# Performance work log

Measured on AMD Instinct MI355X. Metric: run time of the kernel, lower is better.

The kernel has to match this reference:

```python
import jax, jax.numpy as jnp
import numpy as np

# SGCN (AsynSpiGCN) internals are not in the source; reconstructed as a standard
# LIF spiking-GCN: per time step, spikes propagate along edges weighted by
# edge_attr (gather src -> scatter-add dst), membrane potential decays with
# decay_alpha, neurons fire above threshold unless refractory, reset to v_r.
V_REST = 0.0
V_R = 0.0
SPEED = 1.0
THRESH = 0.5
REFRAC = 2.0
DECAY = 0.8
T_STEPS = 8
BETA = 0.5

N_NODES = 50000
N_EDGES = 800000
IN_DIM = 256
HID_DIM = 128


def setup_inputs() -> dict:
    key = jax.random.key(0)
    k1, k2, k3, k4, k5 = jax.random.split(key, 5)
    x = jax.random.normal(k1, (N_NODES, IN_DIM), dtype=jnp.float32)
    spike_node = jax.random.randint(k2, (N_NODES,), 0, 2, dtype=jnp.int32)
    edge_index = jax.random.randint(k3, (2, N_EDGES), 0, N_NODES, dtype=jnp.int32)
    node_indices = jnp.arange(N_NODES, dtype=jnp.int32)
    edge_attr = jax.random.uniform(k4, (N_EDGES,), dtype=jnp.float32)
    W = jax.random.normal(k5, (IN_DIM, HID_DIM), dtype=jnp.float32) * 0.05
    b = jnp.zeros((HID_DIM,), dtype=jnp.float32)
    return {"x": x, "spike_node": spike_node, "edge_index": edge_index,
            "node_indices": node_indices, "edge_attr": edge_attr, "W": W, "b": b}


def reference(x, spike_node, edge_index, node_indices, edge_attr, W, b):
    N = x.shape[0]
    # Linear projection + per-feature min-max standardization over nodes (dim 0)
    h = x @ W + b
    mn = h.min(axis=0, keepdims=True)
    mx = h.max(axis=0, keepdims=True)
    h = (h - mn) / (mx - mn + 1e-6)

    src, dst = edge_index[0], edge_index[1]
    v0 = jnp.full_like(h, V_REST)            # membrane potential [N, H]
    ref0 = jnp.zeros_like(h)                 # refractory counters [N, H]
    s0 = jnp.broadcast_to(spike_node.astype(h.dtype)[:, None], h.shape)

    def step(carry, _):
        v, ref, s = carry
        msg = s[src] * edge_attr[:, None]                      # [E, H] gather
        agg = jax.ops.segment_sum(msg, dst, num_segments=N)    # [N, H] scatter-add
        v = DECAY * v + SPEED * h + agg
        can_fire = ref <= 0
        spk = ((v >= THRESH) & can_fire).astype(h.dtype)
        v = jnp.where(spk > 0, V_R, v)
        ref = jnp.where(spk > 0, REFRAC, jnp.maximum(ref - 1.0, 0.0))
        return (v, ref, spk), spk

    (vT, _, _), spike_matrix = jax.lax.scan(step, (v0, ref0, s0), None, length=T_STEPS)
    fusion_tensor = h + BETA * vT
    return fusion_tensor, spike_matrix
```

## Files before the change

### kernel.cpp

```cpp
#include <hip/hip_runtime.h>
#include <cstdint>

#define N_NODES 50000
#define N_EDGES 800000
#define IN_DIM  256
#define HID     128
#define T_STEPS 8

static __device__ __forceinline__ unsigned int enc_f(float f) {
    unsigned int u = __float_as_uint(f);
    return (u & 0x80000000u) ? ~u : (u | 0x80000000u);
}
static __device__ __forceinline__ float dec_f(unsigned int u) {
    unsigned int b = (u & 0x80000000u) ? (u ^ 0x80000000u) : ~u;
    return __uint_as_float(b);
}

__global__ void k_count(const int* __restrict__ dst, int* __restrict__ counts) {
    int e = blockIdx.x * blockDim.x + threadIdx.x;
    if (e < N_EDGES) atomicAdd(&counts[dst[e]], 1);
}

__global__ void k_scan1(const int* __restrict__ counts, int* __restrict__ row_tmp,
                        int* __restrict__ blocksum) {
    __shared__ int sh[256];
    int t = threadIdx.x, i = blockIdx.x * 256 + t;
    int c = (i < N_NODES) ? counts[i] : 0;
    sh[t] = c; __syncthreads();
    for (int off = 1; off < 256; off <<= 1) {
        int val = (t >= off) ? sh[t - off] : 0;
        __syncthreads();
        sh[t] += val;
        __syncthreads();
    }
    if (i < N_NODES) row_tmp[i] = sh[t] - c;
    if (t == 255) blocksum[blockIdx.x] = sh[255];
}

__global__ void k_scan2(const int* __restrict__ blocksum, int* __restrict__ blockoff,
                        int nb, int* __restrict__ row_ptr) {
    if (threadIdx.x == 0) {
        int acc = 0;
        for (int b = 0; b < nb; ++b) { blockoff[b] = acc; acc += blocksum[b]; }
        row_ptr[N_NODES] = acc;
    }
}

__global__ void k_scan3(const int* __restrict__ row_tmp, const int* __restrict__ blockoff,
                        int* __restrict__ row_ptr) {
    int i = blockIdx.x * blockDim.x + threadIdx.x;
    if (i < N_NODES) row_ptr[i] = row_tmp[i] + blockoff[i >> 8];
}

__global__ void k_fill(const int* __restrict__ dst, const int* __restrict__ src,
                       const float* __restrict__ attr,
                       const int* __restrict__ row_ptr, int* __restrict__ cursor,
                       int* __restrict__ eid, int* __restrict__ src_s,
                       float* __restrict__ attr_s) {
    int e = blockIdx.x * blockDim.x + threadIdx.x;
    if (e >= N_EDGES) return;
    int d = dst[e];
    int p = row_ptr[d] + atomicAdd(&cursor[d], 1);
    eid[p]    = e;
    src_s[p]  = src[e];
    attr_s[p] = attr[e];
}

__global__ __launch_bounds__(256) void k_bsort(const int* __restrict__ row_ptr,
                                               int* __restrict__ eid,
                                               int* __restrict__ src_s,
                                               float* __restrict__ attr_s) {
    int node = blockIdx.x * 4 + (threadIdx.x >> 6);
    int l = threadIdx.x & 63;
    int beg = row_ptr[node], end = row_ptr[node + 1], cnt = end - beg;
    if (cnt <= 1) return;
    if (cnt <= 64) {
        int key = 0x7FFFFFFF, sv = 0; float av = 0.f;
        if (l < cnt) { key = eid[beg + l]; sv = src_s[beg + l]; av = attr_s[beg + l]; }
        #pragma unroll
        for (int k = 2; k <= 64; k <<= 1) {
            for (int j = k >> 1; j > 0; j >>= 1) {
                int   pk = __shfl_xor(key, j);
                int   ps = __shfl_xor(sv, j);
                float pa = __shfl_xor(av, j);
                bool lower = (l & j) == 0;
                bool asc   = (l & k) == 0;
                bool take_min = (lower == asc);
                bool take = take_min ? (pk < key) : (pk > key);
                if (take) { key = pk; sv = ps; av = pa; }
            }
        }
        if (l < cnt) { eid[beg + l] = key; src_s[beg + l] = sv; attr_s[beg + l] = av; }
    } else if (l == 0) {
        for (int i = beg + 1; i < end; ++i) {
            int ke = eid[i]; int ks = src_s[i]; float ka = attr_s[i];
            int m = i - 1;
            while (m >= beg && eid[m] > ke) {
                eid[m+1] = eid[m]; src_s[m+1] = src_s[m]; attr_s[m+1] = attr_s[m]; --m;
            }
            eid[m+1] = ke; src_s[m+1] = ks; attr_s[m+1] = ka;
        }
    }
}

__global__ __launch_bounds__(256) void k_gemm(const float* __restrict__ x,
                                              const float* __restrict__ W,
                                              const float* __restrict__ b,
                                              float* __restrict__ h,
                                              unsigned int* __restrict__ mn_e,
                                              unsigned int* __restrict__ mx_e) {
    __shared__ float Ws[32 * 128];
    __shared__ float xs[64 * 36];
    __shared__ float red_mn[8 * 128];
    __shared__ float red_mx[8 * 128];
    const int tid = threadIdx.x;
    const int n0 = blockIdx.x * 64;
    const int jt = tid & 31, nt = tid >> 5;
    const int j0 = jt * 4;

    float acc[8][4];
    #pragma unroll
    for (int a = 0; a < 8; ++a)
        #pragma unroll
        for (int c = 0; c < 4; ++c) acc[a][c] = 0.0f;

    const int ldn = tid >> 2;
    const int kq  = (tid & 3) * 8;
    const int xrow = (n0 + ldn < N_NODES) ? (n0 + ldn) : (N_NODES - 1);
    const float* xg = x + (size_t)xrow * IN_DIM;

    for (int kc = 0; kc < IN_DIM; kc += 32) {
        __syncthreads();
        float4 xa = *(const float4*)(xg + kc + kq);
        float4 xb = *(const float4*)(xg + kc + kq + 4);
        *(float4*)&xs[ldn * 36 + kq]     = xa;
        *(float4*)&xs[ldn * 36 + kq + 4] = xb;
        #pragma unroll
        for (int p = 0; p < 4; ++p) {
            int r = nt + p * 8;
            *(float4*)&Ws[r * 128 + j0] =
                *(const float4*)(W + (size_t)(kc + r) * HID + j0);
        }
        __syncthreads();
        const float* xbase = &xs[nt * 8 * 36];
        #pragma unroll 4
        for (int k = 0; k < 32; ++k) {
            float4 wf = *(const float4*)&Ws[k * 128 + j0];
            #pragma unroll
            for (int ni = 0; ni < 8; ++ni) {
                float xv = xbase[ni * 36 + k];
                acc[ni][0] = __fmaf_rn(xv, wf.x, acc[ni][0]);
                acc[ni][1] = __fmaf_rn(xv, wf.y, acc[ni][1]);
                acc[ni][2] = __fmaf_rn(xv, wf.z, acc[ni][2]);
                acc[ni][3] = __fmaf_rn(xv, wf.w, acc[ni][3]);
            }
        }
    }

    float4 bv = *(const float4*)(b + j0);
    float lmn[4], lmx[4];
    #pragma unroll
    for (int c = 0; c < 4; ++c) { lmn[c] = INFINITY; lmx[c] = -INFINITY; }
    #pragma unroll
    for (int ni = 0; ni < 8; ++ni) {
        acc[ni][0] = __fadd_rn(acc[ni][0], bv.x);
        acc[ni][1] = __fadd_rn(acc[ni][1], bv.y);
        acc[ni][2] = __fadd_rn(acc[ni][2], bv.z);
        acc[ni][3] = __fadd_rn(acc[ni][3], bv.w);
        #pragma unroll
        for (int c = 0; c < 4; ++c) {
            lmn[c] = fminf(lmn[c], acc[ni][c]);
            lmx[c] = fmaxf(lmx[c], acc[ni][c]);
        }
    }
    #pragma unroll
    for (int c = 0; c < 4; ++c) {
        red_mn[nt * 128 + j0 + c] = lmn[c];
        red_mx[nt * 128 + j0 + c] = lmx[c];
    }
    __syncthreads();
    if (tid < 128) {
        float mnv = red_mn[tid], mxv = red_mx[tid];
        #pragma unroll
        for (int r = 1; r < 8; ++r) {
            mnv = fminf(mnv, red_mn[r * 128 + tid]);
            mxv = fmaxf(mxv, red_mx[r * 128 + tid]);
        }
        atomicMin(&mn_e[tid], enc_f(mnv));
        atomicMax(&mx_e[tid], enc_f(mxv));
    }
    #pragma unroll
    for (int ni = 0; ni < 8; ++ni) {
        int n = n0 + nt * 8 + ni;
        if (n < N_NODES)
            *(float4*)&h[(size_t)n * HID + j0] =
                make_float4(acc[ni][0], acc[ni][1], acc[ni][2], acc[ni][3]);
    }
}

__global__ void k_init_bits(const int* __restrict__ spike_node, uint32_t* __restrict__ sb) {
    int n = blockIdx.x * blockDim.x + threadIdx.x;
    if (n >= N_NODES) return;
    uint32_t f = spike_node[n] ? 0xFFFFFFFFu : 0u;
    sb[(size_t)n * 4 + 0] = f;
    sb[(size_t)n * 4 + 1] = f;
    sb[(size_t)n * 4 + 2] = f;
    sb[(size_t)n * 4 + 3] = f;
}

__global__ __launch_bounds__(128) void k_step(const int* __restrict__ row_ptr,
                                              const int* __restrict__ src_s,
                                              const float* __restrict__ attr_s,
                                              const uint32_t* __restrict__ sb_cur,
                                              uint32_t* __restrict__ sb_nxt,
                                              float* __restrict__ h,
                                              float* __restrict__ v,
                                              unsigned char* __restrict__ refc,
                                              const unsigned int* __restrict__ mn_e,
                                              const unsigned int* __restrict__ mx_e,
                                              float* __restrict__ out_spk,
                                              float* __restrict__ out_fus,
                                              int t0, int is_last) {
    __shared__ float    attr_l[4][128];
    __shared__ uint32_t words_l[4][128][4];
    __shared__ uint32_t sbw[16];
    __shared__ int      rp[5];

    const int tid = threadIdx.x;
    const int ns = tid >> 5, ln = tid & 31;
    const int nb = blockIdx.x * 4;
    const int n  = nb + ns;

    if (tid < 16) sbw[tid] = 0;
    if (tid < 5)  rp[tid] = row_ptr[nb + tid];
    __syncthreads();

    const int beg = rp[ns], cnt = rp[ns + 1] - beg;
    int cmax = 0;
    #pragma unroll
    for (int q = 0; q < 4; ++q) cmax = max(cmax, rp[q + 1] - rp[q]);
    const int nchunk = (cmax + 127) >> 7;

    float agg0 = 0.f, agg1 = 0.f, agg2 = 0.f, agg3 = 0.f;
    const int w = ln >> 3, shb = (ln & 7) * 4;

    for (int ch = 0; ch < nchunk; ++ch) {
        int base = ch << 7;
        __syncthreads();
        #pragma unroll
        for (int rep = 0; rep < 4; ++rep) {
            int i = base + rep * 32 + ln;
            if (i < cnt) {
                int e = beg + i;
                int s = src_s[e];
                attr_l[ns][rep * 32 + ln] = attr_s[e];
                *(uint4*)&words_l[ns][rep * 32 + ln][0] =
                    *(const uint4*)&sb_cur[(size_t)s * 4];
            }
        }
        __syncthreads();
        int lim = min(128, cnt - base);
        for (int i = 0; i < lim; ++i) {
            uint32_t u = words_l[ns][i][w];
            float a = attr_l[ns][i];
            uint32_t bits = (u >> shb) & 0xFu;
            agg0 = __fadd_rn(agg0, (bits & 1u) ? a : 0.0f);
            agg1 = __fadd_rn(agg1, (bits & 2u) ? a : 0.0f);
            agg2 = __fadd_rn(agg2, (bits & 4u) ? a : 0.0f);
            agg3 = __fadd_rn(agg3, (bits & 8u) ? a : 0.0f);
        }
    }

    const size_t idx = (size_t)n * HID + ln * 4;
    float4 h4 = *(const float4*)&h[idx];
    if (t0) {
        const int jb = ln * 4;
        float hq[4] = {h4.x, h4.y, h4.z, h4.w};
        #pragma unroll
        for (int q = 0; q < 4; ++q) {
            float mn = dec_f(mn_e[jb + q]);
            float mx = dec_f(mx_e[jb + q]);
            float d2 = __fadd_rn(__fsub_rn(mx, mn), 1e-6f);
            hq[q] = __fdiv_rn(__fsub_rn(hq[q], mn), d2);
        }
        h4 = make_float4(hq[0], hq[1], hq[2], hq[3]);
        *(float4*)&h[idx] = h4;
    }
    float4 v4;
    unsigned int rcu;
    if (t0) { v4 = make_float4(0.f, 0.f, 0.f, 0.f); rcu = 0u; }
    else    { v4 = *(const float4*)&v[idx]; rcu = *(const unsigned int*)&refc[idx]; }

    float hv[4]  = {h4.x, h4.y, h4.z, h4.w};
    float vv[4]  = {v4.x, v4.y, v4.z, v4.w};
    float ag[4]  = {agg0, agg1, agg2, agg3};
    float vf[4], sf[4];
    unsigned int rcn = 0u, nib = 0u;
    #pragma unroll
    for (int q = 0; q < 4; ++q) {
        float vn = __fadd_rn(__fadd_rn(__fmul_rn(0.8f, vv[q]), hv[q]), ag[q]);
        unsigned int rc = (rcu >> (8 * q)) & 0xFFu;
        bool spk = (vn >= 0.5f) && (rc == 0u);
        vf[q] = spk ? 0.0f : vn;
        sf[q] = spk ? 1.0f : 0.0f;
        unsigned int rnew = spk ? 2u : (rc > 0u ? rc - 1u : 0u);
        rcn |= rnew << (8 * q);
        nib |= (spk ? 1u : 0u) << q;
    }
    *(float4*)&v[idx] = make_float4(vf[0], vf[1], vf[2], vf[3]);
    *(unsigned int*)&refc[idx] = rcn;
    *(float4*)&out_spk[idx] = make_float4(sf[0], sf[1], sf[2], sf[3]);
    if (is_last) {
        *(float4*)&out_fus[idx] = make_float4(
            __fadd_rn(hv[0], __fmul_rn(0.5f, vf[0])),
            __fadd_rn(hv[1], __fmul_rn(0.5f, vf[1])),
            __fadd_rn(hv[2], __fmul_rn(0.5f, vf[2])),
            __fadd_rn(hv[3], __fmul_rn(0.5f, vf[3])));
    }
    atomicOr(&sbw[ns * 4 + w], nib << shb);
    __syncthreads();
    if (tid < 16)
        sb_nxt[(size_t)(nb + (tid >> 2)) * 4 + (tid & 3)] = sbw[tid];
}

extern "C" void kernel_launch(void* const* d_in, const int* in_sizes, int n_in,
                              void* d_out, int out_size, void* d_ws, size_t ws_size,
                              hipStream_t stream) {
    const float* x          = (const float*)d_in[0];
    const int*   spike_node = (const int*)  d_in[1];
    const int*   edge_index = (const int*)  d_in[2];
    const float* edge_attr  = (const float*)d_in[4];
    const float* W          = (const float*)d_in[5];
    const float* b          = (const float*)d_in[6];
    float* out = (float*)d_out;

    const int* src = edge_index;
    const int* dst = edge_index + N_EDGES;

    char* wsp = (char*)d_ws;
    auto alloc = [&](size_t bytes) {
        char* p = wsp;
        wsp += (bytes + 255) & ~(size_t)255;
        return p;
    };
    float*         h        = (float*)        alloc((size_t)N_NODES * HID * 4);
    float*         v        = (float*)        alloc((size_t)N_NODES * HID * 4);
    unsigned char* refc     = (unsigned char*)alloc((size_t)N_NODES * HID);
    uint32_t*      sbA      = (uint32_t*)     alloc((size_t)N_NODES * 16);
    uint32_t*      sbB      = (uint32_t*)     alloc((size_t)N_NODES * 16);
    int*           counts   = (int*)          alloc((size_t)N_NODES * 4);
    int*           cursor   = (int*)          alloc((size_t)N_NODES * 4);
    int*           row_tmp  = (int*)          alloc((size_t)N_NODES * 4);
    int*           row_ptr  = (int*)          alloc((size_t)(N_NODES + 1) * 4);
    int*           blocksum = (int*)          alloc(256 * 4);
    int*           blockoff = (int*)          alloc(256 * 4);
    int*           eid      = (int*)          alloc((size_t)N_EDGES * 4);
    int*           src_s    = (int*)          alloc((size_t)N_EDGES * 4);
    float*         attr_s   = (float*)        alloc((size_t)N_EDGES * 4);
    unsigned int*  mn_e     = (unsigned int*) alloc(HID * 4);
    unsigned int*  mx_e     = (unsigned int*) alloc(HID * 4);

    hipMemsetAsync(counts, 0x00, (size_t)N_NODES * 4, stream);
    hipMemsetAsync(cursor, 0x00, (size_t)N_NODES * 4, stream);
    hipMemsetAsync(mn_e,   0xFF, HID * 4, stream);
    hipMemsetAsync(mx_e,   0x00, HID * 4, stream);

    const int NB = (N_NODES + 255) / 256;
    const int EB = (N_EDGES + 255) / 256;

    k_count<<<EB, 256, 0, stream>>>(dst, counts);
    k_scan1<<<NB, 256, 0, stream>>>(counts, row_tmp, blocksum);
    k_scan2<<<1, 64, 0, stream>>>(blocksum, blockoff, NB, row_ptr);
    k_scan3<<<NB, 256, 0, stream>>>(row_tmp, blockoff, row_ptr);
    k_fill<<<EB, 256, 0, stream>>>(dst, src, edge_attr, row_ptr, cursor, eid, src_s, attr_s);
    k_bsort<<<N_NODES / 4, 256, 0, stream>>>(row_ptr, eid, src_s, attr_s);

    k_gemm<<<(N_NODES + 63) / 64, 256, 0, stream>>>(x, W, b, h, mn_e, mx_e);
    k_init_bits<<<NB, 256, 0, stream>>>(spike_node, sbA);

    const size_t NH = (size_t)N_NODES * HID;
    for (int t = 0; t < T_STEPS; ++t) {
        uint32_t* cur = (t & 1) ? sbB : sbA;
        uint32_t* nxt = (t & 1) ? sbA : sbB;
        k_step<<<N_NODES / 4, 128, 0, stream>>>(row_ptr, src_s, attr_s, cur, nxt,
                                                h, v, refc, mn_e, mx_e,
                                                out + NH + (size_t)t * NH,
                                                out, (t == 0) ? 1 : 0,
                                                (t == T_STEPS - 1) ? 1 : 0);
    }
}
```

Before: 640.9 us.

## Fuse all spiking time steps into one persistent cooperative kernel

Replaces the eight per-step launches with one cooperative kernel that runs every LIF time step and uses grid.sync between steps. Each block owns 66 nodes and keeps their normalized h, membrane potential and refractory counters in registers. Its CSR edge slice is cached in LDS when it fits, so v, refc and h are no longer re-read from and written back to global memory each step. The cost is seven grid-wide barriers and a residency requirement that all ~758 blocks fit at once; if the occupancy check or the cooperative launch fails, the old per-step loop runs instead.

```diff
diff --git a/kernel.cpp b/kernel.cpp
--- a/kernel.cpp
+++ b/kernel.cpp
@@ -1,5 +1,8 @@
 #include <hip/hip_runtime.h>
+#include <hip/hip_cooperative_groups.h>
 #include <cstdint>
+
+namespace cg = cooperative_groups;
 
 #define N_NODES 50000
 #define N_EDGES 800000
@@ -321,6 +324,186 @@
     __syncthreads();
     if (tid < 16)
         sb_nxt[(size_t)(nb + (tid >> 2)) * 4 + (tid & 3)] = sbw[tid];
+}
+
+#define NPB 66
+#define ECAP 2048
+#define NSLOT 9
+#define GRID_F ((N_NODES + NPB - 1) / NPB)
+__global__ __launch_bounds__(256, 3) void k_fused(
+    const int* __restrict__ row_ptr,
+    const int* __restrict__ src_s,
+    const float* __restrict__ attr_s,
+    uint32_t* __restrict__ sbA,
+    uint32_t* __restrict__ sbB,
+    const float* __restrict__ h_raw,
+    const unsigned int* __restrict__ mn_e,
+    const unsigned int* __restrict__ mx_e,
+    float* __restrict__ out)
+{
+    __shared__ int      lrp[NPB + 1];
+    __shared__ int      ed_src[ECAP];
+    __shared__ float    ed_attr[ECAP];
+    __shared__ uint32_t sbw[NPB][4];
+
+    cg::grid_group grid = cg::this_grid();
+
+    const int tid = threadIdx.x;
+    const int g   = tid >> 5;
+    const int ln  = tid & 31;
+    const int n0  = blockIdx.x * NPB;
+    const int ncnt = (N_NODES - n0 < NPB) ? (N_NODES - n0) : NPB;
+    const int nwords = (ncnt > 0 ? ncnt : 0) * 4;
+    const int w = ln >> 3, shb = (ln & 7) * 4;
+    const size_t NH = (size_t)N_NODES * HID;
+
+    int ebase = 0; bool inlds = false;
+    if (ncnt > 0) {
+        if (tid <= ncnt) lrp[tid] = row_ptr[n0 + tid];
+        __syncthreads();
+        ebase = lrp[0];
+        int etot = lrp[ncnt] - ebase;
+        inlds = (etot <= ECAP);
+        if (inlds) {
+            for (int i = tid; i < etot; i += 256) {
+                ed_src[i]  = src_s[ebase + i];
+                ed_attr[i] = attr_s[ebase + i];
+            }
+        }
+    }
+    __syncthreads();
+
+    uint4 mnu = *(const uint4*)&mn_e[ln * 4];
+    uint4 mxu = *(const uint4*)&mx_e[ln * 4];
+    float mn0 = dec_f(mnu.x), mn1 = dec_f(mnu.y), mn2 = dec_f(mnu.z), mn3 = dec_f(mnu.w);
+    float dd0 = __fadd_rn(__fsub_rn(dec_f(mxu.x), mn0), 1e-6f);
+    float dd1 = __fadd_rn(__fsub_rn(dec_f(mxu.y), mn1), 1e-6f);
+    float dd2 = __fadd_rn(__fsub_rn(dec_f(mxu.z), mn2), 1e-6f);
+    float dd3 = __fadd_rn(__fsub_rn(dec_f(mxu.w), mn3), 1e-6f);
+
+    float4 hs[NSLOT], vs[NSLOT];
+    uint32_t rcs[NSLOT];
+    #pragma unroll
+    for (int s = 0; s < NSLOT; ++s) {
+        hs[s] = make_float4(0.f, 0.f, 0.f, 0.f);
+        vs[s] = make_float4(0.f, 0.f, 0.f, 0.f);
+        rcs[s] = 0u;
+        int m = s * 8 + g;
+        if (m < ncnt) {
+            size_t idx = (size_t)(n0 + m) * HID + ln * 4;
+            float4 t = *(const float4*)&h_raw[idx];
+            t.x = __fdiv_rn(__fsub_rn(t.x, mn0), dd0);
+            t.y = __fdiv_rn(__fsub_rn(t.y, mn1), dd1);
+            t.z = __fdiv_rn(__fsub_rn(t.z, mn2), dd2);
+            t.w = __fdiv_rn(__fsub_rn(t.w, mn3), dd3);
+            hs[s] = t;
+        }
+    }
+
+    for (int t = 0; t < T_STEPS; ++t) {
+        const uint32_t* cur = (t & 1) ? sbB : sbA;
+        uint32_t*       nxt = (t & 1) ? sbA : sbB;
+        if (t > 0) {
+            __threadfence();
+            grid.sync();
+            __threadfence();
+        }
+        for (int i2 = tid; i2 < nwords; i2 += 256) ((uint32_t*)sbw)[i2] = 0u;
+        __syncthreads();
+
+        #pragma unroll 1
+        for (int s = 0; s < NSLOT; ++s) {
+            int m = s * 8 + g;
+            if (m >= ncnt) continue;
+            int lb, le;
+            if (inlds) { lb = lrp[m] - ebase; le = lrp[m + 1] - ebase; }
+            else       { lb = lrp[m];         le = lrp[m + 1]; }
+            float ag0 = 0.f, ag1 = 0.f, ag2 = 0.f, ag3 = 0.f;
+            int i = lb;
+            if (inlds) {
+                for (; i + 3 < le; i += 4) {
+                    int e0 = ed_src[i], e1 = ed_src[i+1], e2 = ed_src[i+2], e3 = ed_src[i+3];
+                    uint32_t u0 = cur[(size_t)e0 * 4 + w];
+                    uint32_t u1 = cur[(size_t)e1 * 4 + w];
+                    uint32_t u2 = cur[(size_t)e2 * 4 + w];
+                    uint32_t u3 = cur[(size_t)e3 * 4 + w];
+                    float a0 = ed_attr[i], a1 = ed_attr[i+1], a2 = ed_attr[i+2], a3 = ed_attr[i+3];
+                    uint32_t b0 = (u0 >> shb) & 0xFu, b1 = (u1 >> shb) & 0xFu;
+                    uint32_t b2 = (u2 >> shb) & 0xFu, b3 = (u3 >> shb) & 0xFu;
+                    ag0 = __fadd_rn(ag0, (b0 & 1u) ? a0 : 0.f);
+                    ag1 = __fadd_rn(ag1, (b0 & 2u) ? a0 : 0.f);
+                    ag2 = __fadd_rn(ag2, (b0 & 4u) ? a0 : 0.f);
+                    ag3 = __fadd_rn(ag3, (b0 & 8u) ? a0 : 0.f);
+                    ag0 = __fadd_rn(ag0, (b1 & 1u) ? a1 : 0.f);
+                    ag1 = __fadd_rn(ag1, (b1 & 2u) ? a1 : 0.f);
+                    ag2 = __fadd_rn(ag2, (b1 & 4u) ? a1 : 0.f);
+                    ag3 = __fadd_rn(ag3, (b1 & 8u) ? a1 : 0.f);
+                    ag0 = __fadd_rn(ag0, (b2 & 1u) ? a2 : 0.f);
+                    ag1 = __fadd_rn(ag1, (b2 & 2u) ? a2 : 0.f);
+                    ag2 = __fadd_rn(ag2, (b2 & 4u) ? a2 : 0.f);
+                    ag3 = __fadd_rn(ag3, (b2 & 8u) ? a2 : 0.f);
+                    ag0 = __fadd_rn(ag0, (b3 & 1u) ? a3 : 0.f);
+                    ag1 = __fadd_rn(ag1, (b3 & 2u) ? a3 : 0.f);
+                    ag2 = __fadd_rn(ag2, (b3 & 4u) ? a3 : 0.f);
+                    ag3 = __fadd_rn(ag3, (b3 & 8u) ? a3 : 0.f);
+                }
+                for (; i < le; ++i) {
+                    int e0 = ed_src[i];
+                    uint32_t u0 = cur[(size_t)e0 * 4 + w];
+                    float a0 = ed_attr[i];
+                    uint32_t b0 = (u0 >> shb) & 0xFu;
+                    ag0 = __fadd_rn(ag0, (b0 & 1u) ? a0 : 0.f);
+                    ag1 = __fadd_rn(ag1, (b0 & 2u) ? a0 : 0.f);
+                    ag2 = __fadd_rn(ag2, (b0 & 4u) ? a0 : 0.f);
+                    ag3 = __fadd_rn(ag3, (b0 & 8u) ? a0 : 0.f);
+                }
+            } else {
+                for (; i < le; ++i) {
+                    int e0 = src_s[i];
+                    uint32_t u0 = cur[(size_t)e0 * 4 + w];
+                    float a0 = attr_s[i];
+                    uint32_t b0 = (u0 >> shb) & 0xFu;
+                    ag0 = __fadd_rn(ag0, (b0 & 1u) ? a0 : 0.f);
+                    ag1 = __fadd_rn(ag1, (b0 & 2u) ? a0 : 0.f);
+                    ag2 = __fadd_rn(ag2, (b0 & 4u) ? a0 : 0.f);
+                    ag3 = __fadd_rn(ag3, (b0 & 8u) ? a0 : 0.f);
+                }
+            }
+
+            float hv[4] = {hs[s].x, hs[s].y, hs[s].z, hs[s].w};
+            float vv[4] = {vs[s].x, vs[s].y, vs[s].z, vs[s].w};
+            float ag[4] = {ag0, ag1, ag2, ag3};
+            float vf[4], sf[4];
+            uint32_t rcu = rcs[s], rcn = 0u, nib = 0u;
+            #pragma unroll
+            for (int q = 0; q < 4; ++q) {
+                float vn = __fadd_rn(__fadd_rn(__fmul_rn(0.8f, vv[q]), hv[q]), ag[q]);
+                uint32_t rc = (rcu >> (8 * q)) & 0xFFu;
+                bool spk = (vn >= 0.5f) && (rc == 0u);
+                vf[q] = spk ? 0.0f : vn;
+                sf[q] = spk ? 1.0f : 0.0f;
+                uint32_t rnew = spk ? 2u : (rc > 0u ? rc - 1u : 0u);
+                rcn |= rnew << (8 * q);
+                nib |= (spk ? 1u : 0u) << q;
+            }
+            vs[s] = make_float4(vf[0], vf[1], vf[2], vf[3]);
+            rcs[s] = rcn;
+            size_t idx = (size_t)(n0 + m) * HID + ln * 4;
+            *(float4*)&out[NH + (size_t)t * NH + idx] =
+                make_float4(sf[0], sf[1], sf[2], sf[3]);
+            if (t == T_STEPS - 1) {
+                *(float4*)&out[idx] = make_float4(
+                    __fadd_rn(hv[0], __fmul_rn(0.5f, vf[0])),
+                    __fadd_rn(hv[1], __fmul_rn(0.5f, vf[1])),
+                    __fadd_rn(hv[2], __fmul_rn(0.5f, vf[2])),
+                    __fadd_rn(hv[3], __fmul_rn(0.5f, vf[3])));
+            }
+            atomicOr(&sbw[m][w], nib << shb);
+        }
+        __syncthreads();
+        for (int i2 = tid; i2 < nwords; i2 += 256)
+            nxt[(size_t)n0 * 4 + i2] = ((uint32_t*)sbw)[i2];
+    }
 }
 
 extern "C" void kernel_launch(void* const* d_in, const int* in_sizes, int n_in,
@@ -379,13 +562,37 @@
     k_init_bits<<<NB, 256, 0, stream>>>(spike_node, sbA);
 
     const size_t NH = (size_t)N_NODES * HID;
-    for (int t = 0; t < T_STEPS; ++t) {
-        uint32_t* cur = (t & 1) ? sbB : sbA;
-        uint32_t* nxt = (t & 1) ? sbA : sbB;
-        k_step<<<N_NODES / 4, 128, 0, stream>>>(row_ptr, src_s, attr_s, cur, nxt,
-                                                h, v, refc, mn_e, mx_e,
-                                                out + NH + (size_t)t * NH,
-                                                out, (t == 0) ? 1 : 0,
-                                                (t == T_STEPS - 1) ? 1 : 0);
-    }
-}
+
+    int maxB = 0;
+    hipError_t qerr = hipOccupancyMaxActiveBlocksPerMultiprocessor(&maxB, k_fused, 256, 0);
+    bool coop_done = false;
+    if (qerr == hipSuccess && maxB * 256 >= GRID_F) {
+        const int*          a_row  = row_ptr;
+        const int*          a_src  = src_s;
+        const float*        a_attr = attr_s;
+        uint32_t*           a_sbA  = sbA;
+        uint32_t*           a_sbB  = sbB;
+        const float*        a_h    = h;
+        const unsigned int* a_mn   = mn_e;
+        const unsigned int* a_mx   = mx_e;
+        float*              a_out  = out;
+        void* kargs[] = { (void*)&a_row, (void*)&a_src, (void*)&a_attr,
+                          (void*)&a_sbA, (void*)&a_sbB, (void*)&a_h,
+                          (void*)&a_mn,  (void*)&a_mx,  (void*)&a_out };
+        hipError_t lerr = hipLaunchCooperativeKernel((const void*)k_fused,
+                                                     dim3(GRID_F), dim3(256),
+                                                     kargs, 0, stream);
+        coop_done = (lerr == hipSuccess);
+    }
+    if (!coop_done) {
+        for (int t = 0; t < T_STEPS; ++t) {
+            uint32_t* cur = (t & 1) ? sbB : sbA;
+            uint32_t* nxt = (t & 1) ? sbA : sbB;
+            k_step<<<N_NODES / 4, 128, 0, stream>>>(row_ptr, src_s, attr_s, cur, nxt,
+                                                    h, v, refc, mn_e, mx_e,
+                                                    out + NH + (size_t)t * NH,
+                                                    out, (t == 0) ? 1 : 0,
+                                                    (t == T_STEPS - 1) ? 1 : 0);
+        }
+    }
+}
```

New measurement: 2.307 ms. 260% more time.

## Fuse all LIF time steps into one persistent kernel with grid barrier

Applied to the files above, without the earlier changes.

Replaces eight per-step kernel launches with a single persistent kernel of about 511 blocks. Each block owns 98 nodes and keeps h, v and refractory state in registers across steps. The block's edge lists are cached in LDS once, and steps are separated by a software global barrier built on atomics. This removes the global-memory round trips of v and refc, the repeated edge-list loads, and the launch overhead. The grid barrier depends on every block being co-resident (256 threads, launch_bounds 2 blocks/CU, heavy LDS and register use), so it risks deadlock or spilling, and the barrier adds serialization per step.

```diff
diff --git a/kernel.cpp b/kernel.cpp
--- a/kernel.cpp
+++ b/kernel.cpp
@@ -208,119 +208,176 @@
     sb[(size_t)n * 4 + 3] = f;
 }
 
-__global__ __launch_bounds__(128) void k_step(const int* __restrict__ row_ptr,
-                                              const int* __restrict__ src_s,
-                                              const float* __restrict__ attr_s,
-                                              const uint32_t* __restrict__ sb_cur,
-                                              uint32_t* __restrict__ sb_nxt,
-                                              float* __restrict__ h,
-                                              float* __restrict__ v,
-                                              unsigned char* __restrict__ refc,
-                                              const unsigned int* __restrict__ mn_e,
-                                              const unsigned int* __restrict__ mx_e,
-                                              float* __restrict__ out_spk,
-                                              float* __restrict__ out_fus,
-                                              int t0, int is_last) {
-    __shared__ float    attr_l[4][128];
-    __shared__ uint32_t words_l[4][128][4];
-    __shared__ uint32_t sbw[16];
-    __shared__ int      rp[5];
+static __device__ __forceinline__ void gbar(int* cnt, int* gen, int nblk) {
+    __syncthreads();
+    if (threadIdx.x == 0) {
+        __threadfence();
+        int g = __hip_atomic_load(gen, __ATOMIC_RELAXED, __HIP_MEMORY_SCOPE_AGENT);
+        int arrived = __hip_atomic_fetch_add(cnt, 1, __ATOMIC_ACQ_REL,
+                                             __HIP_MEMORY_SCOPE_AGENT);
+        if (arrived == nblk - 1) {
+            __hip_atomic_store(cnt, 0, __ATOMIC_RELAXED, __HIP_MEMORY_SCOPE_AGENT);
+            __threadfence();
+            __hip_atomic_fetch_add(gen, 1, __ATOMIC_ACQ_REL, __HIP_MEMORY_SCOPE_AGENT);
+        } else {
+            while (__hip_atomic_load(gen, __ATOMIC_RELAXED,
+                                     __HIP_MEMORY_SCOPE_AGENT) == g)
+                __builtin_amdgcn_s_sleep(16);
+        }
+        __threadfence();
+    }
+    __syncthreads();
+}
+
+#define NPB   98
+#define NSLOT 13
+#define ECAP  2048
+#define GRID_P ((N_NODES + NPB - 1) / NPB)
+__global__ __launch_bounds__(256, 2) void k_lif(
+    const int* __restrict__ row_ptr,
+    const int* __restrict__ src_s,
+    const float* __restrict__ attr_s,
+    uint32_t* __restrict__ sbA,
+    uint32_t* __restrict__ sbB,
+    const float* __restrict__ h_raw,
+    const unsigned int* __restrict__ mn_e,
+    const unsigned int* __restrict__ mx_e,
+    float* __restrict__ out,
+    int* __restrict__ bar_cnt,
+    int* __restrict__ bar_gen)
+{
+    __shared__ int      lrp[NPB + 1];
+    __shared__ int      ed_src_l[ECAP];
+    __shared__ float    ed_attr_l[ECAP];
+    __shared__ uint32_t ed_wds[ECAP * 4];
+    __shared__ uint32_t sbw[NPB][4];
 
     const int tid = threadIdx.x;
-    const int ns = tid >> 5, ln = tid & 31;
-    const int nb = blockIdx.x * 4;
-    const int n  = nb + ns;
-
-    if (tid < 16) sbw[tid] = 0;
-    if (tid < 5)  rp[tid] = row_ptr[nb + tid];
+    const int g   = tid >> 5;
+    const int ln  = tid & 31;
+    const int n0  = blockIdx.x * NPB;
+    const int ncnt = min(NPB, N_NODES - n0);
+    const int w = ln >> 3, shb = (ln & 7) * 4;
+    const size_t NH = (size_t)N_NODES * HID;
+
+    if (tid <= ncnt) lrp[tid] = row_ptr[n0 + tid];
     __syncthreads();
-
-    const int beg = rp[ns], cnt = rp[ns + 1] - beg;
-    int cmax = 0;
-    #pragma unroll
-    for (int q = 0; q < 4; ++q) cmax = max(cmax, rp[q + 1] - rp[q]);
-    const int nchunk = (cmax + 127) >> 7;
-
-    float agg0 = 0.f, agg1 = 0.f, agg2 = 0.f, agg3 = 0.f;
-    const int w = ln >> 3, shb = (ln & 7) * 4;
-
-    for (int ch = 0; ch < nchunk; ++ch) {
-        int base = ch << 7;
-        __syncthreads();
-        #pragma unroll
-        for (int rep = 0; rep < 4; ++rep) {
-            int i = base + rep * 32 + ln;
-            if (i < cnt) {
-                int e = beg + i;
-                int s = src_s[e];
-                attr_l[ns][rep * 32 + ln] = attr_s[e];
-                *(uint4*)&words_l[ns][rep * 32 + ln][0] =
-                    *(const uint4*)&sb_cur[(size_t)s * 4];
+    const int ebase = lrp[0];
+    const int etot  = lrp[ncnt] - ebase;
+    const bool inlds = (etot <= ECAP);
+    if (inlds) {
+        for (int i = tid; i < etot; i += 256) {
+            ed_src_l[i]  = src_s[ebase + i];
+            ed_attr_l[i] = attr_s[ebase + i];
+        }
+    }
+
+    uint4 mnu = *(const uint4*)&mn_e[ln * 4];
+    uint4 mxu = *(const uint4*)&mx_e[ln * 4];
+    float mn0 = dec_f(mnu.x), mn1 = dec_f(mnu.y), mn2 = dec_f(mnu.z), mn3 = dec_f(mnu.w);
+    float dd0 = __fadd_rn(__fsub_rn(dec_f(mxu.x), mn0), 1e-6f);
+    float dd1 = __fadd_rn(__fsub_rn(dec_f(mxu.y), mn1), 1e-6f);
+    float dd2 = __fadd_rn(__fsub_rn(dec_f(mxu.z), mn2), 1e-6f);
+    float dd3 = __fadd_rn(__fsub_rn(dec_f(mxu.w), mn3), 1e-6f);
+
+    float4 hs[NSLOT], vs[NSLOT];
+    uint32_t rcs[NSLOT];
+    #pragma unroll
+    for (int s = 0; s < NSLOT; ++s) {
+        hs[s] = make_float4(0.f, 0.f, 0.f, 0.f);
+        vs[s] = make_float4(0.f, 0.f, 0.f, 0.f);
+        rcs[s] = 0u;
+        int m = s * 8 + g;
+        if (m < ncnt) {
+            size_t idx = (size_t)(n0 + m) * HID + ln * 4;
+            float4 t = *(const float4*)&h_raw[idx];
+            t.x = __fdiv_rn(__fsub_rn(t.x, mn0), dd0);
+            t.y = __fdiv_rn(__fsub_rn(t.y, mn1), dd1);
+            t.z = __fdiv_rn(__fsub_rn(t.z, mn2), dd2);
+            t.w = __fdiv_rn(__fsub_rn(t.w, mn3), dd3);
+            hs[s] = t;
+        }
+    }
+    __syncthreads();
+
+    for (int t = 0; t < T_STEPS; ++t) {
+        const uint32_t* cur = (t & 1) ? sbB : sbA;
+        uint32_t*       nxt = (t & 1) ? sbA : sbB;
+        if (t > 0) gbar(bar_cnt, bar_gen, GRID_P);
+
+        for (int i = tid; i < ncnt * 4; i += 256) ((uint32_t*)sbw)[i] = 0u;
+        if (inlds) {
+            for (int i = tid; i < etot; i += 256) {
+                int s = ed_src_l[i];
+                *(uint4*)&ed_wds[i * 4] = *(const uint4*)&cur[(size_t)s * 4];
             }
         }
         __syncthreads();
-        int lim = min(128, cnt - base);
-        for (int i = 0; i < lim; ++i) {
-            uint32_t u = words_l[ns][i][w];
-            float a = attr_l[ns][i];
-            uint32_t bits = (u >> shb) & 0xFu;
-            agg0 = __fadd_rn(agg0, (bits & 1u) ? a : 0.0f);
-            agg1 = __fadd_rn(agg1, (bits & 2u) ? a : 0.0f);
-            agg2 = __fadd_rn(agg2, (bits & 4u) ? a : 0.0f);
-            agg3 = __fadd_rn(agg3, (bits & 8u) ? a : 0.0f);
-        }
-    }
-
-    const size_t idx = (size_t)n * HID + ln * 4;
-    float4 h4 = *(const float4*)&h[idx];
-    if (t0) {
-        const int jb = ln * 4;
-        float hq[4] = {h4.x, h4.y, h4.z, h4.w};
-        #pragma unroll
-        for (int q = 0; q < 4; ++q) {
-            float mn = dec_f(mn_e[jb + q]);
-            float mx = dec_f(mx_e[jb + q]);
-            float d2 = __fadd_rn(__fsub_rn(mx, mn), 1e-6f);
-            hq[q] = __fdiv_rn(__fsub_rn(hq[q], mn), d2);
-        }
-        h4 = make_float4(hq[0], hq[1], hq[2], hq[3]);
-        *(float4*)&h[idx] = h4;
-    }
-    float4 v4;
-    unsigned int rcu;
-    if (t0) { v4 = make_float4(0.f, 0.f, 0.f, 0.f); rcu = 0u; }
-    else    { v4 = *(const float4*)&v[idx]; rcu = *(const unsigned int*)&refc[idx]; }
-
-    float hv[4]  = {h4.x, h4.y, h4.z, h4.w};
-    float vv[4]  = {v4.x, v4.y, v4.z, v4.w};
-    float ag[4]  = {agg0, agg1, agg2, agg3};
-    float vf[4], sf[4];
-    unsigned int rcn = 0u, nib = 0u;
-    #pragma unroll
-    for (int q = 0; q < 4; ++q) {
-        float vn = __fadd_rn(__fadd_rn(__fmul_rn(0.8f, vv[q]), hv[q]), ag[q]);
-        unsigned int rc = (rcu >> (8 * q)) & 0xFFu;
-        bool spk = (vn >= 0.5f) && (rc == 0u);
-        vf[q] = spk ? 0.0f : vn;
-        sf[q] = spk ? 1.0f : 0.0f;
-        unsigned int rnew = spk ? 2u : (rc > 0u ? rc - 1u : 0u);
-        rcn |= rnew << (8 * q);
-        nib |= (spk ? 1u : 0u) << q;
-    }
-    *(float4*)&v[idx] = make_float4(vf[0], vf[1], vf[2], vf[3]);
-    *(unsigned int*)&refc[idx] = rcn;
-    *(float4*)&out_spk[idx] = make_float4(sf[0], sf[1], sf[2], sf[3]);
-    if (is_last) {
-        *(float4*)&out_fus[idx] = make_float4(
-            __fadd_rn(hv[0], __fmul_rn(0.5f, vf[0])),
-            __fadd_rn(hv[1], __fmul_rn(0.5f, vf[1])),
-            __fadd_rn(hv[2], __fmul_rn(0.5f, vf[2])),
-            __fadd_rn(hv[3], __fmul_rn(0.5f, vf[3])));
-    }
-    atomicOr(&sbw[ns * 4 + w], nib << shb);
-    __syncthreads();
-    if (tid < 16)
-        sb_nxt[(size_t)(nb + (tid >> 2)) * 4 + (tid & 3)] = sbw[tid];
+
+        #pragma unroll
+        for (int s = 0; s < NSLOT; ++s) {
+            int m = s * 8 + g;
+            if (m < ncnt) {
+                float ag0 = 0.f, ag1 = 0.f, ag2 = 0.f, ag3 = 0.f;
+                if (inlds) {
+                    int lb = lrp[m] - ebase, le = lrp[m + 1] - ebase;
+                    for (int i = lb; i < le; ++i) {
+                        uint32_t u = ed_wds[i * 4 + w];
+                        float a = ed_attr_l[i];
+                        uint32_t bits = (u >> shb) & 0xFu;
+                        ag0 = __fadd_rn(ag0, (bits & 1u) ? a : 0.f);
+                        ag1 = __fadd_rn(ag1, (bits & 2u) ? a : 0.f);
+                        ag2 = __fadd_rn(ag2, (bits & 4u) ? a : 0.f);
+                        ag3 = __fadd_rn(ag3, (bits & 8u) ? a : 0.f);
+                    }
+                } else {
+                    int lb = lrp[m], le = lrp[m + 1];
+                    for (int i = lb; i < le; ++i) {
+                        uint32_t u = cur[(size_t)src_s[i] * 4 + w];
+                        float a = attr_s[i];
+                        uint32_t bits = (u >> shb) & 0xFu;
+                        ag0 = __fadd_rn(ag0, (bits & 1u) ? a : 0.f);
+                        ag1 = __fadd_rn(ag1, (bits & 2u) ? a : 0.f);
+                        ag2 = __fadd_rn(ag2, (bits & 4u) ? a : 0.f);
+                        ag3 = __fadd_rn(ag3, (bits & 8u) ? a : 0.f);
+                    }
+                }
+
+                float hv[4] = {hs[s].x, hs[s].y, hs[s].z, hs[s].w};
+                float vv[4] = {vs[s].x, vs[s].y, vs[s].z, vs[s].w};
+                float ag[4] = {ag0, ag1, ag2, ag3};
+                float vf[4], sf[4];
+                uint32_t rcu = rcs[s], rcn = 0u, nib = 0u;
+                #pragma unroll
+                for (int q = 0; q < 4; ++q) {
+                    float vn = __fadd_rn(__fadd_rn(__fmul_rn(0.8f, vv[q]), hv[q]), ag[q]);
+                    uint32_t rc = (rcu >> (8 * q)) & 0xFFu;
+                    bool spk = (vn >= 0.5f) && (rc == 0u);
+                    vf[q] = spk ? 0.0f : vn;
+                    sf[q] = spk ? 1.0f : 0.0f;
+                    uint32_t rnew = spk ? 2u : (rc > 0u ? rc - 1u : 0u);
+                    rcn |= rnew << (8 * q);
+                    nib |= (spk ? 1u : 0u) << q;
+                }
+                vs[s] = make_float4(vf[0], vf[1], vf[2], vf[3]);
+                rcs[s] = rcn;
+                size_t idx = (size_t)(n0 + m) * HID + ln * 4;
+                *(float4*)&out[NH + (size_t)t * NH + idx] =
+                    make_float4(sf[0], sf[1], sf[2], sf[3]);
+                if (t == T_STEPS - 1) {
+                    *(float4*)&out[idx] = make_float4(
+                        __fadd_rn(hv[0], __fmul_rn(0.5f, vf[0])),
+                        __fadd_rn(hv[1], __fmul_rn(0.5f, vf[1])),
+                        __fadd_rn(hv[2], __fmul_rn(0.5f, vf[2])),
+                        __fadd_rn(hv[3], __fmul_rn(0.5f, vf[3])));
+                }
+                atomicOr(&sbw[m][w], nib << shb);
+            }
+        }
+        __syncthreads();
+        for (int i = tid; i < ncnt * 4; i += 256)
+            nxt[(size_t)n0 * 4 + i] = ((uint32_t*)sbw)[i];
+    }
 }
 
 extern "C" void kernel_launch(void* const* d_in, const int* in_sizes, int n_in,
@@ -344,8 +401,6 @@
         return p;
     };
     float*         h        = (float*)        alloc((size_t)N_NODES * HID * 4);
-    float*         v        = (float*)        alloc((size_t)N_NODES * HID * 4);
-    unsigned char* refc     = (unsigned char*)alloc((size_t)N_NODES * HID);
     uint32_t*      sbA      = (uint32_t*)     alloc((size_t)N_NODES * 16);
     uint32_t*      sbB      = (uint32_t*)     alloc((size_t)N_NODES * 16);
     int*           counts   = (int*)          alloc((size_t)N_NODES * 4);
@@ -359,11 +414,13 @@
     float*         attr_s   = (float*)        alloc((size_t)N_EDGES * 4);
     unsigned int*  mn_e     = (unsigned int*) alloc(HID * 4);
     unsigned int*  mx_e     = (unsigned int*) alloc(HID * 4);
+    int*           barv     = (int*)          alloc(256);
 
     hipMemsetAsync(counts, 0x00, (size_t)N_NODES * 4, stream);
     hipMemsetAsync(cursor, 0x00, (size_t)N_NODES * 4, stream);
     hipMemsetAsync(mn_e,   0xFF, HID * 4, stream);
     hipMemsetAsync(mx_e,   0x00, HID * 4, stream);
+    hipMemsetAsync(barv,   0x00, 256, stream);
 
     const int NB = (N_NODES + 255) / 256;
     const int EB = (N_EDGES + 255) / 256;
@@ -378,14 +435,6 @@
     k_gemm<<<(N_NODES + 63) / 64, 256, 0, stream>>>(x, W, b, h, mn_e, mx_e);
     k_init_bits<<<NB, 256, 0, stream>>>(spike_node, sbA);
 
-    const size_t NH = (size_t)N_NODES * HID;
-    for (int t = 0; t < T_STEPS; ++t) {
-        uint32_t* cur = (t & 1) ? sbB : sbA;
-        uint32_t* nxt = (t & 1) ? sbA : sbB;
-        k_step<<<N_NODES / 4, 128, 0, stream>>>(row_ptr, src_s, attr_s, cur, nxt,
-                                                h, v, refc, mn_e, mx_e,
-                                                out + NH + (size_t)t * NH,
-                                                out, (t == 0) ? 1 : 0,
-                                                (t == T_STEPS - 1) ? 1 : 0);
-    }
-}
+    k_lif<<<GRID_P, 256, 0, stream>>>(row_ptr, src_s, attr_s, sbA, sbB,
+                                      h, mn_e, mx_e, out, &barv[0], &barv[1]);
+}
```

Measured after the change: 1.100 ms. +71.6%, slower.

## Fuse all LIF time steps into one persistent kernel with grid barrier

Applied to the files above, without the earlier changes.

Replaces the eight per-step k_step launches with a single persistent kernel that keeps h, v and refractory state in registers and caches each block's edge list in LDS. Time steps are separated by a hierarchical software grid barrier built on atomics, chosen only when occupancy lets the whole grid be resident. Edge src and attr are packed into one int2 array so each edge needs one load. This removes per-step launch overhead and the global-memory traffic for v, refc and h, at the cost of relying on co-residency for the spin barrier and serialising on barrier latency.

```diff
diff --git a/kernel.cpp b/kernel.cpp
--- a/kernel.cpp
+++ b/kernel.cpp
@@ -55,34 +55,31 @@
 __global__ void k_fill(const int* __restrict__ dst, const int* __restrict__ src,
                        const float* __restrict__ attr,
                        const int* __restrict__ row_ptr, int* __restrict__ cursor,
-                       int* __restrict__ eid, int* __restrict__ src_s,
-                       float* __restrict__ attr_s) {
+                       int* __restrict__ eid, int2* __restrict__ edata) {
     int e = blockIdx.x * blockDim.x + threadIdx.x;
     if (e >= N_EDGES) return;
     int d = dst[e];
     int p = row_ptr[d] + atomicAdd(&cursor[d], 1);
-    eid[p]    = e;
-    src_s[p]  = src[e];
-    attr_s[p] = attr[e];
+    eid[p]   = e;
+    edata[p] = make_int2(src[e], __float_as_int(attr[e]));
 }
 
 __global__ __launch_bounds__(256) void k_bsort(const int* __restrict__ row_ptr,
                                                int* __restrict__ eid,
-                                               int* __restrict__ src_s,
-                                               float* __restrict__ attr_s) {
+                                               int2* __restrict__ edata) {
     int node = blockIdx.x * 4 + (threadIdx.x >> 6);
     int l = threadIdx.x & 63;
     int beg = row_ptr[node], end = row_ptr[node + 1], cnt = end - beg;
     if (cnt <= 1) return;
     if (cnt <= 64) {
-        int key = 0x7FFFFFFF, sv = 0; float av = 0.f;
-        if (l < cnt) { key = eid[beg + l]; sv = src_s[beg + l]; av = attr_s[beg + l]; }
+        int key = 0x7FFFFFFF, sv = 0, av = 0;
+        if (l < cnt) { key = eid[beg + l]; int2 d = edata[beg + l]; sv = d.x; av = d.y; }
         #pragma unroll
         for (int k = 2; k <= 64; k <<= 1) {
             for (int j = k >> 1; j > 0; j >>= 1) {
-                int   pk = __shfl_xor(key, j);
-                int   ps = __shfl_xor(sv, j);
-                float pa = __shfl_xor(av, j);
+                int pk = __shfl_xor(key, j);
+                int ps = __shfl_xor(sv, j);
+                int pa = __shfl_xor(av, j);
                 bool lower = (l & j) == 0;
                 bool asc   = (l & k) == 0;
                 bool take_min = (lower == asc);
@@ -90,15 +87,15 @@
                 if (take) { key = pk; sv = ps; av = pa; }
             }
         }
-        if (l < cnt) { eid[beg + l] = key; src_s[beg + l] = sv; attr_s[beg + l] = av; }
+        if (l < cnt) { eid[beg + l] = key; edata[beg + l] = make_int2(sv, av); }
     } else if (l == 0) {
         for (int i = beg + 1; i < end; ++i) {
-            int ke = eid[i]; int ks = src_s[i]; float ka = attr_s[i];
+            int ke = eid[i]; int2 kd = edata[i];
             int m = i - 1;
             while (m >= beg && eid[m] > ke) {
-                eid[m+1] = eid[m]; src_s[m+1] = src_s[m]; attr_s[m+1] = attr_s[m]; --m;
+                eid[m+1] = eid[m]; edata[m+1] = edata[m]; --m;
             }
-            eid[m+1] = ke; src_s[m+1] = ks; attr_s[m+1] = ka;
+            eid[m+1] = ke; edata[m+1] = kd;
         }
     }
 }
@@ -208,9 +205,210 @@
     sb[(size_t)n * 4 + 3] = f;
 }
 
+static __device__ __forceinline__ void gbar2(int* bar, int nblk) {
+    __syncthreads();
+    if (threadIdx.x == 0) {
+        __threadfence();
+        const int l   = blockIdx.x & 7;
+        const int lsz = (nblk - l + 7) >> 3;
+        int* lc = bar + l * 64;
+        int* lg = bar + 512 + l * 64;
+        int* rc = bar + 1024;
+        int* rg = bar + 1088;
+        int gl = __hip_atomic_load(lg, __ATOMIC_RELAXED, __HIP_MEMORY_SCOPE_AGENT);
+        int a  = __hip_atomic_fetch_add(lc, 1, __ATOMIC_ACQ_REL, __HIP_MEMORY_SCOPE_AGENT);
+        if (a == lsz - 1) {
+            __hip_atomic_store(lc, 0, __ATOMIC_RELAXED, __HIP_MEMORY_SCOPE_AGENT);
+            int gr = __hip_atomic_load(rg, __ATOMIC_RELAXED, __HIP_MEMORY_SCOPE_AGENT);
+            int r  = __hip_atomic_fetch_add(rc, 1, __ATOMIC_ACQ_REL, __HIP_MEMORY_SCOPE_AGENT);
+            if (r == 7) {
+                __hip_atomic_store(rc, 0, __ATOMIC_RELAXED, __HIP_MEMORY_SCOPE_AGENT);
+                __hip_atomic_fetch_add(rg, 1, __ATOMIC_ACQ_REL, __HIP_MEMORY_SCOPE_AGENT);
+            } else {
+                while (__hip_atomic_load(rg, __ATOMIC_RELAXED,
+                                         __HIP_MEMORY_SCOPE_AGENT) == gr)
+                    __builtin_amdgcn_s_sleep(4);
+            }
+            __hip_atomic_fetch_add(lg, 1, __ATOMIC_ACQ_REL, __HIP_MEMORY_SCOPE_AGENT);
+        } else {
+            while (__hip_atomic_load(lg, __ATOMIC_RELAXED,
+                                     __HIP_MEMORY_SCOPE_AGENT) == gl)
+                __builtin_amdgcn_s_sleep(8);
+        }
+        __threadfence();
+    }
+    __syncthreads();
+}
+
+template<int TNPB, int TNSLOT, int TECAP, int TPACK, int TMINW>
+__global__ __launch_bounds__(256, TMINW) void k_lif_t(
+    const int* __restrict__ row_ptr,
+    const int2* __restrict__ edata,
+    uint32_t* __restrict__ sbA,
+    uint32_t* __restrict__ sbB,
+    const float* __restrict__ h_raw,
+    const unsigned int* __restrict__ mn_e,
+    const unsigned int* __restrict__ mx_e,
+    float* __restrict__ out,
+    int* __restrict__ bar,
+    int nblk)
+{
+    __shared__ int      lrp[TNPB + 1];
+    __shared__ int      ed_src_l[TECAP];
+    __shared__ float    ed_attr_l[TECAP];
+    __shared__ uint32_t ed_wds[TPACK ? 1 : TECAP * 4];
+    __shared__ uint2    ed_pk[TPACK ? TECAP * 4 : 1];
+    __shared__ uint32_t sbw[TNPB][4];
+
+    const int tid = threadIdx.x;
+    const int g   = tid >> 5;
+    const int ln  = tid & 31;
+    const int n0  = blockIdx.x * TNPB;
+    const int ncnt = min(TNPB, N_NODES - n0);
+    const int w = ln >> 3, shb = (ln & 7) * 4;
+    const size_t NH = (size_t)N_NODES * HID;
+
+    if (tid <= ncnt) lrp[tid] = row_ptr[n0 + tid];
+    __syncthreads();
+    const int ebase = lrp[0];
+    const int etot  = lrp[ncnt] - ebase;
+    const bool inlds = (etot <= TECAP);
+    if (inlds) {
+        for (int i = tid; i < etot; i += 256) {
+            int2 d = edata[ebase + i];
+            ed_src_l[i]  = d.x;
+            ed_attr_l[i] = __int_as_float(d.y);
+        }
+    }
+
+    uint4 mnu = *(const uint4*)&mn_e[ln * 4];
+    uint4 mxu = *(const uint4*)&mx_e[ln * 4];
+    float mn0 = dec_f(mnu.x), mn1 = dec_f(mnu.y), mn2 = dec_f(mnu.z), mn3 = dec_f(mnu.w);
+    float dd0 = __fadd_rn(__fsub_rn(dec_f(mxu.x), mn0), 1e-6f);
+    float dd1 = __fadd_rn(__fsub_rn(dec_f(mxu.y), mn1), 1e-6f);
+    float dd2 = __fadd_rn(__fsub_rn(dec_f(mxu.z), mn2), 1e-6f);
+    float dd3 = __fadd_rn(__fsub_rn(dec_f(mxu.w), mn3), 1e-6f);
+
+    float4 hs[TNSLOT], vs[TNSLOT];
+    uint32_t rcs[TNSLOT];
+    #pragma unroll
+    for (int s = 0; s < TNSLOT; ++s) {
+        hs[s] = make_float4(0.f, 0.f, 0.f, 0.f);
+        vs[s] = make_float4(0.f, 0.f, 0.f, 0.f);
+        rcs[s] = 0u;
+        int m = s * 8 + g;
+        if (m < ncnt) {
+            size_t idx = (size_t)(n0 + m) * HID + ln * 4;
+            float4 t = *(const float4*)&h_raw[idx];
+            t.x = __fdiv_rn(__fsub_rn(t.x, mn0), dd0);
+            t.y = __fdiv_rn(__fsub_rn(t.y, mn1), dd1);
+            t.z = __fdiv_rn(__fsub_rn(t.z, mn2), dd2);
+            t.w = __fdiv_rn(__fsub_rn(t.w, mn3), dd3);
+            hs[s] = t;
+        }
+    }
+    for (int i = tid; i < ncnt * 4; i += 256) ((uint32_t*)sbw)[i] = 0u;
+    __syncthreads();
+
+    for (int t = 0; t < T_STEPS; ++t) {
+        const uint32_t* cur = (t & 1) ? sbB : sbA;
+        uint32_t*       nxt = (t & 1) ? sbA : sbB;
+        if (t > 0) gbar2(bar, nblk);
+
+        if (inlds) {
+            for (int i = tid; i < etot; i += 256) {
+                uint4 wv = *(const uint4*)&cur[(size_t)ed_src_l[i] * 4];
+                if (TPACK) {
+                    uint32_t ab = __float_as_uint(ed_attr_l[i]);
+                    ed_pk[i * 4 + 0] = make_uint2(ab, wv.x);
+                    ed_pk[i * 4 + 1] = make_uint2(ab, wv.y);
+                    ed_pk[i * 4 + 2] = make_uint2(ab, wv.z);
+                    ed_pk[i * 4 + 3] = make_uint2(ab, wv.w);
+                } else {
+                    *(uint4*)&ed_wds[i * 4] = wv;
+                }
+            }
+        }
+        __syncthreads();
+
+        #pragma unroll
+        for (int s = 0; s < TNSLOT; ++s) {
+            int m = s * 8 + g;
+            if (m < ncnt) {
+                float ag0 = 0.f, ag1 = 0.f, ag2 = 0.f, ag3 = 0.f;
+                if (inlds) {
+                    int lb = lrp[m] - ebase, le = lrp[m + 1] - ebase;
+                    for (int i = lb; i < le; ++i) {
+                        uint32_t u; float a;
+                        if (TPACK) {
+                            uint2 p = ed_pk[i * 4 + w];
+                            a = __uint_as_float(p.x);
+                            u = p.y;
+                        } else {
+                            u = ed_wds[i * 4 + w];
+                            a = ed_attr_l[i];
+                        }
+                        uint32_t bits = (u >> shb) & 0xFu;
+                        ag0 = __fadd_rn(ag0, (bits & 1u) ? a : 0.f);
+                        ag1 = __fadd_rn(ag1, (bits & 2u) ? a : 0.f);
+                        ag2 = __fadd_rn(ag2, (bits & 4u) ? a : 0.f);
+                        ag3 = __fadd_rn(ag3, (bits & 8u) ? a : 0.f);
+                    }
+                } else {
+                    int lb = lrp[m], le = lrp[m + 1];
+                    for (int i = lb; i < le; ++i) {
+                        int2 d = edata[i];
+                        uint32_t u = cur[(size_t)d.x * 4 + w];
+                        float a = __int_as_float(d.y);
+                        uint32_t bits = (u >> shb) & 0xFu;
+                        ag0 = __fadd_rn(ag0, (bits & 1u) ? a : 0.f);
+                        ag1 = __fadd_rn(ag1, (bits & 2u) ? a : 0.f);
+                        ag2 = __fadd_rn(ag2, (bits & 4u) ? a : 0.f);
+                        ag3 = __fadd_rn(ag3, (bits & 8u) ? a : 0.f);
+                    }
+                }
+
+                float hv[4] = {hs[s].x, hs[s].y, hs[s].z, hs[s].w};
+                float vv[4] = {vs[s].x, vs[s].y, vs[s].z, vs[s].w};
+                float ag[4] = {ag0, ag1, ag2, ag3};
+                float vf[4], sf[4];
+                uint32_t rcu = rcs[s], rcn = 0u, nib = 0u;
+                #pragma unroll
+                for (int q = 0; q < 4; ++q) {
+                    float vn = __fadd_rn(__fadd_rn(__fmul_rn(0.8f, vv[q]), hv[q]), ag[q]);
+                    uint32_t rc = (rcu >> (8 * q)) & 0xFFu;
+                    bool spk = (vn >= 0.5f) && (rc == 0u);
+                    vf[q] = spk ? 0.0f : vn;
+                    sf[q] = spk ? 1.0f : 0.0f;
+                    uint32_t rnew = spk ? 2u : (rc > 0u ? rc - 1u : 0u);
+                    rcn |= rnew << (8 * q);
+                    nib |= (spk ? 1u : 0u) << q;
+                }
+                vs[s] = make_float4(vf[0], vf[1], vf[2], vf[3]);
+                rcs[s] = rcn;
+                size_t idx = (size_t)(n0 + m) * HID + ln * 4;
+                *(float4*)&out[NH + (size_t)t * NH + idx] =
+                    make_float4(sf[0], sf[1], sf[2], sf[3]);
+                if (t == T_STEPS - 1) {
+                    *(float4*)&out[idx] = make_float4(
+                        __fadd_rn(hv[0], __fmul_rn(0.5f, vf[0])),
+                        __fadd_rn(hv[1], __fmul_rn(0.5f, vf[1])),
+                        __fadd_rn(hv[2], __fmul_rn(0.5f, vf[2])),
+                        __fadd_rn(hv[3], __fmul_rn(0.5f, vf[3])));
+                }
+                atomicOr(&sbw[m][w], nib << shb);
+            }
+        }
+        __syncthreads();
+        for (int i = tid; i < ncnt * 4; i += 256) {
+            nxt[(size_t)n0 * 4 + i] = ((uint32_t*)sbw)[i];
+            ((uint32_t*)sbw)[i] = 0u;
+        }
+    }
+}
+
 __global__ __launch_bounds__(128) void k_step(const int* __restrict__ row_ptr,
-                                              const int* __restrict__ src_s,
-                                              const float* __restrict__ attr_s,
+                                              const int2* __restrict__ edata,
                                               const uint32_t* __restrict__ sb_cur,
                                               uint32_t* __restrict__ sb_nxt,
                                               float* __restrict__ h,
@@ -251,11 +449,10 @@
         for (int rep = 0; rep < 4; ++rep) {
             int i = base + rep * 32 + ln;
             if (i < cnt) {
-                int e = beg + i;
-                int s = src_s[e];
-                attr_l[ns][rep * 32 + ln] = attr_s[e];
+                int2 d = edata[beg + i];
+                attr_l[ns][rep * 32 + ln] = __int_as_float(d.y);
                 *(uint4*)&words_l[ns][rep * 32 + ln][0] =
-                    *(const uint4*)&sb_cur[(size_t)s * 4];
+                    *(const uint4*)&sb_cur[(size_t)d.x * 4];
             }
         }
         __syncthreads();
@@ -355,15 +552,16 @@
     int*           blocksum = (int*)          alloc(256 * 4);
     int*           blockoff = (int*)          alloc(256 * 4);
     int*           eid      = (int*)          alloc((size_t)N_EDGES * 4);
-    int*           src_s    = (int*)          alloc((size_t)N_EDGES * 4);
-    float*         attr_s   = (float*)        alloc((size_t)N_EDGES * 4);
+    int2*          edata    = (int2*)         alloc((size_t)N_EDGES * 8);
     unsigned int*  mn_e     = (unsigned int*) alloc(HID * 4);
     unsigned int*  mx_e     = (unsigned int*) alloc(HID * 4);
+    int*           barv     = (int*)          alloc(8192);
 
     hipMemsetAsync(counts, 0x00, (size_t)N_NODES * 4, stream);
     hipMemsetAsync(cursor, 0x00, (size_t)N_NODES * 4, stream);
     hipMemsetAsync(mn_e,   0xFF, HID * 4, stream);
     hipMemsetAsync(mx_e,   0x00, HID * 4, stream);
+    hipMemsetAsync(barv,   0x00, 8192, stream);
 
     const int NB = (N_NODES + 255) / 256;
     const int EB = (N_EDGES + 255) / 256;
@@ -372,20 +570,37 @@
     k_scan1<<<NB, 256, 0, stream>>>(counts, row_tmp, blocksum);
     k_scan2<<<1, 64, 0, stream>>>(blocksum, blockoff, NB, row_ptr);
     k_scan3<<<NB, 256, 0, stream>>>(row_tmp, blockoff, row_ptr);
-    k_fill<<<EB, 256, 0, stream>>>(dst, src, edge_attr, row_ptr, cursor, eid, src_s, attr_s);
-    k_bsort<<<N_NODES / 4, 256, 0, stream>>>(row_ptr, eid, src_s, attr_s);
+    k_fill<<<EB, 256, 0, stream>>>(dst, src, edge_attr, row_ptr, cursor, eid, edata);
+    k_bsort<<<N_NODES / 4, 256, 0, stream>>>(row_ptr, eid, edata);
 
     k_gemm<<<(N_NODES + 63) / 64, 256, 0, stream>>>(x, W, b, h, mn_e, mx_e);
     k_init_bits<<<NB, 256, 0, stream>>>(spike_node, sbA);
 
     const size_t NH = (size_t)N_NODES * HID;
-    for (int t = 0; t < T_STEPS; ++t) {
-        uint32_t* cur = (t & 1) ? sbB : sbA;
-        uint32_t* nxt = (t & 1) ? sbA : sbB;
-        k_step<<<N_NODES / 4, 128, 0, stream>>>(row_ptr, src_s, attr_s, cur, nxt,
-                                                h, v, refc, mn_e, mx_e,
-                                                out + NH + (size_t)t * NH,
-                                                out, (t == 0) ? 1 : 0,
-                                                (t == T_STEPS - 1) ? 1 : 0);
-    }
-}
+
+    auto kA = k_lif_t<66, 9, 1536, 0, 3>;
+    auto kB = k_lif_t<98, 13, 1920, 1, 2>;
+    int occA = 0, occB = 0;
+    hipOccupancyMaxActiveBlocksPerMultiprocessor(&occA, kA, 256, 0);
+    hipOccupancyMaxActiveBlocksPerMultiprocessor(&occB, kB, 256, 0);
+
+    if (occA >= 3) {
+        const int grid = (N_NODES + 65) / 66;
+        kA<<<grid, 256, 0, stream>>>(row_ptr, edata, sbA, sbB, h, mn_e, mx_e,
+                                     out, barv, grid);
+    } else if (occB >= 2) {
+        const int grid = (N_NODES + 97) / 98;
+        kB<<<grid, 256, 0, stream>>>(row_ptr, edata, sbA, sbB, h, mn_e, mx_e,
+                                     out, barv, grid);
+    } else {
+        for (int t = 0; t < T_STEPS; ++t) {
+            uint32_t* cur = (t & 1) ? sbB : sbA;
+            uint32_t* nxt = (t & 1) ? sbA : sbB;
+            k_step<<<N_NODES / 4, 128, 0, stream>>>(row_ptr, edata, cur, nxt,
+                                                    h, v, refc, mn_e, mx_e,
+                                                    out + NH + (size_t)t * NH,
+                                                    out, (t == 0) ? 1 : 0,
+                                                    (t == T_STEPS - 1) ? 1 : 0);
+        }
+    }
+}
```

After: 624.7 us. 1.03x faster.
